# Optimization experiments

Hardware: AMD Instinct MI355X
Metric: run time of the kernel (lower is better)

Reference implementation:

```python
import jax, jax.numpy as jnp
import numpy as np

N = 8192
D_IN = 1024
D_OUT = 1024


def setup_inputs() -> dict:
    key = jax.random.key(0)
    k1, k2, k3, k4 = jax.random.split(key, 4)
    # param scales mimic reset_parameters: weight ~ U(-r, r), transfers ~ N(0, 0.001)
    r = np.sqrt(6.0 / (D_IN + D_OUT))
    x = jax.random.normal(k1, (N, D_IN), dtype=jnp.float32)
    weight = jax.random.uniform(k2, (D_IN, D_OUT), dtype=jnp.float32, minval=-r, maxval=r)
    transferi = jax.random.normal(k3, (D_IN, D_IN), dtype=jnp.float32) * 0.001
    transferj = jax.random.normal(k4, (D_IN, D_IN), dtype=jnp.float32) * 0.001
    return {"x": x, "weight": weight, "transferi": transferi, "transferj": transferj}


def reference(x, weight, transferi, transferj):
    # support = x @ W  -> [N, out]
    support = x @ weight
    # NOTE: the original torch code uses transferi for BOTH projections (transferj unused)
    x_i = x @ transferi            # [N, in]
    x_j = x @ transferi            # [N, in]
    scores = x_i @ x_j.T           # [N, N] inner-product attention, no scaling
    attn = jax.nn.softmax(scores, axis=1)
    return attn @ support          # [N, out]
```

## Files before the change

### kernel.cpp

```cpp
#include <hip/hip_runtime.h>
#include <hip/hip_bf16.h>
#include <cstddef>

#define NQ 8192
#define DD 1024

typedef __attribute__((ext_vector_type(8))) short s8v;
typedef __attribute__((ext_vector_type(8))) int i8v;
typedef __attribute__((ext_vector_type(4))) float f32x4;
typedef __attribute__((ext_vector_type(16))) float f32x16;

typedef const __attribute__((address_space(1))) unsigned int* gptr_t;
typedef __attribute__((address_space(3))) unsigned int* lptr_t;

#define SCALE_1_16 0x7B7B7B7Bu

__device__ inline unsigned short f2bf(float f) {
  union { float f; unsigned u; } v; v.f = f;
  unsigned r = (v.u + 0x7FFFu + ((v.u >> 16) & 1u)) >> 16;
  return (unsigned short)r;
}
__device__ inline float bits2f(unsigned u) {
  union { unsigned u; float f; } v; v.u = u;
  return v.f;
}

__device__ inline unsigned char f2e4m3(float x) {
  union { float f; unsigned u; } v; v.f = x;
  const unsigned s = (v.u >> 31) << 7;
  unsigned au = v.u & 0x7FFFFFFFu;
  if (au > 0x43E00000u) au = 0x43E00000u;
  if (au >= 0x3C800000u) {
    const unsigned rounded = au + 0x7FFFFu + ((au >> 20) & 1u);
    const unsigned e8 = ((rounded >> 23) & 0xFF) - 120u;
    const unsigned m8 = (rounded >> 20) & 7u;
    return (unsigned char)(s | (e8 << 3) | m8);
  } else {
    union { unsigned u; float f; } a; a.u = au;
    const unsigned q = (unsigned)rintf(a.f * 512.0f);
    return (unsigned char)(s | q);
  }
}

__device__ inline i8v make_i8v(int4 a, int4 b) {
  i8v v;
  v[0] = a.x; v[1] = a.y; v[2] = a.z; v[3] = a.w;
  v[4] = b.x; v[5] = b.y; v[6] = b.z; v[7] = b.w;
  return v;
}

template <int KDIM, int ASTR, int BSTR>
__device__ inline void mfma_core(const unsigned short* __restrict__ A,
                                 const unsigned short* __restrict__ B,
                                 int i0, int j0, int tid,
                                 unsigned short* AsU, unsigned short* BsU,
                                 f32x4 (&acc)[4][4]) {
  const int lane = tid & 63;
  const int w = tid >> 6;
  const int wr = (w >> 1) * 64;
  const int wc = (w & 1) * 64;
  const int l16 = lane & 15;
  const int lq = lane >> 4;
  const int srow = lane >> 3;
  const int scol = (((lane & 7) ^ (srow & 7)) * 8);

  for (int kk = 0; kk < KDIM; kk += 64) {
    __syncthreads();
#pragma unroll
    for (int t = 0; t < 4; t++) {
      const int r0 = w * 32 + t * 8;
      const unsigned short* g = &A[(size_t)(i0 + r0 + srow) * ASTR + kk + scol];
      __builtin_amdgcn_global_load_lds((gptr_t)(const void*)g,
                                       (lptr_t)(void*)&AsU[r0 * 64], 16, 0, 0);
    }
#pragma unroll
    for (int t = 0; t < 4; t++) {
      const int r0 = w * 32 + t * 8;
      const unsigned short* g = &B[(size_t)(j0 + r0 + srow) * BSTR + kk + scol];
      __builtin_amdgcn_global_load_lds((gptr_t)(const void*)g,
                                       (lptr_t)(void*)&BsU[r0 * 64], 16, 0, 0);
    }
    __syncthreads();

    const int h = l16 & 7;
    s8v af[4][2], bf[4][2];
#pragma unroll
    for (int t = 0; t < 4; t++)
#pragma unroll
      for (int s = 0; s < 2; s++) {
        const int ch = ((s * 4 + lq) ^ h) * 8;
        af[t][s] = *(const s8v*)&AsU[(wr + 16 * t + l16) * 64 + ch];
        bf[t][s] = *(const s8v*)&BsU[(wc + 16 * t + l16) * 64 + ch];
      }
#pragma unroll
    for (int s = 0; s < 2; s++)
#pragma unroll
      for (int a = 0; a < 4; a++)
#pragma unroll
        for (int b = 0; b < 4; b++)
          acc[a][b] = __builtin_amdgcn_mfma_f32_16x16x32_bf16(
              af[a][s], bf[b][s], acc[a][b], 0, 0, 0);
  }
}

__global__ void f32_to_bf16(const float* __restrict__ in,
                            unsigned short* __restrict__ out, int n4) {
  int i = (blockIdx.x * blockDim.x + threadIdx.x);
  if (i < n4) {
    const float4 v = *(const float4*)&in[i * 4];
    ushort4 o;
    o.x = f2bf(v.x); o.y = f2bf(v.y); o.z = f2bf(v.z); o.w = f2bf(v.w);
    *(ushort4*)&out[i * 4] = o;
  }
}

__global__ void zero_f32(float* __restrict__ p, int n) {
  const int i = blockIdx.x * blockDim.x + threadIdx.x;
  if (i < n) p[i] = 0.f;
}

__global__ void zero_f32v4(float* __restrict__ p, int n4) {
  const int i = blockIdx.x * blockDim.x + threadIdx.x;
  if (i < n4) *(float4*)&p[i * 4] = (float4){0.f, 0.f, 0.f, 0.f};
}

__global__ void transpose_cvt(const float* __restrict__ in,
                              unsigned short* __restrict__ out, int R, int C) {
  __shared__ float t[32][33];
  const int bx = blockIdx.x;
  const int by = blockIdx.y;
  const int x = threadIdx.x & 31;
  const int y = threadIdx.x >> 5;
#pragma unroll
  for (int i = 0; i < 32; i += 8)
    t[y + i][x] = in[(size_t)(by * 32 + y + i) * C + bx * 32 + x];
  __syncthreads();
#pragma unroll
  for (int i = 0; i < 32; i += 8)
    out[(size_t)(bx * 32 + y + i) * R + by * 32 + x] = f2bf(t[x][y + i]);
}

template <int NST, bool FP8OUT>
__global__ __launch_bounds__(256, 2)
void proj_gemm(const unsigned short* __restrict__ A,
               const unsigned short* __restrict__ BT,
               void* __restrict__ Cout) {
  __shared__ __align__(16) unsigned short As[128 * 64];
  __shared__ __align__(16) unsigned short Bs[128 * 64];
  const int tid = threadIdx.x;
  const int m0 = blockIdx.y * 128;
  const int n0 = blockIdx.x * 128;

  f32x4 acc[4][4];
#pragma unroll
  for (int a = 0; a < 4; a++)
#pragma unroll
    for (int b = 0; b < 4; b++) acc[a][b] = (f32x4){0.f, 0.f, 0.f, 0.f};

  mfma_core<DD, DD, DD>(A, BT, m0, n0, tid, As, Bs, acc);

  const int lane = tid & 63;
  const int w = tid >> 6;
  const int wr = (w >> 1) * 64, wc = (w & 1) * 64;
  const int l16 = lane & 15, lq = lane >> 4;
#pragma unroll
  for (int ti = 0; ti < 4; ti++)
#pragma unroll
    for (int r = 0; r < 4; r++) {
      const int row = m0 + wr + 16 * ti + lq * 4 + r;
#pragma unroll
      for (int tj = 0; tj < 4; tj++) {
        const int col = n0 + wc + 16 * tj + l16;
        if (FP8OUT) {
          ((unsigned char*)Cout)[(size_t)row * NST + col] =
              f2e4m3(acc[ti][tj][r] * 16.f);
        } else {
          ((unsigned short*)Cout)[(size_t)row * NST + col] = f2bf(acc[ti][tj][r]);
        }
      }
    }
}

__global__ __launch_bounds__(256, 3)
void qk_fp8(const unsigned char* __restrict__ xif,
            unsigned short* __restrict__ P,
            float* __restrict__ lsum) {
  __shared__ __align__(16) unsigned char AsF[128 * 64];
  __shared__ __align__(16) unsigned char BsF[128 * 64];
  __shared__ float lsums[128][65];
  const int tid = threadIdx.x;
  const int lane = tid & 63;
  const int w = tid >> 6;
  const int i0 = blockIdx.y * 128;
  const int j0 = blockIdx.x * 128;

  f32x16 acc[2][2];
#pragma unroll
  for (int a = 0; a < 2; a++)
#pragma unroll
    for (int b = 0; b < 2; b++)
#pragma unroll
      for (int r = 0; r < 16; r++) acc[a][b][r] = 0.f;

  const int srow = lane >> 2;
  const int slot = lane & 3;
  const int kb = lane >> 5;
  const int l31 = lane & 31;

  for (int kk = 0; kk < DD; kk += 64) {
    __syncthreads();
#pragma unroll
    for (int t = 0; t < 2; t++) {
      const int r = w * 32 + t * 16 + srow;
      const int c = slot ^ ((r >> 1) & 3);
      const unsigned char* ga = &xif[(size_t)(i0 + r) * DD + kk + c * 16];
      const unsigned char* gb = &xif[(size_t)(j0 + r) * DD + kk + c * 16];
      __builtin_amdgcn_global_load_lds((gptr_t)(const void*)ga,
                                       (lptr_t)(void*)&AsF[(w * 32 + t * 16) * 64],
                                       16, 0, 0);
      __builtin_amdgcn_global_load_lds((gptr_t)(const void*)gb,
                                       (lptr_t)(void*)&BsF[(w * 32 + t * 16) * 64],
                                       16, 0, 0);
    }
    __syncthreads();

    i8v af[2], bf[2];
#pragma unroll
    for (int mi = 0; mi < 2; mi++) {
      const int ar = (w >> 1) * 64 + mi * 32 + l31;
      const int sw = (ar >> 1) & 3;
      const int4 q0 = *(const int4*)&AsF[ar * 64 + ((2 * kb + 0) ^ sw) * 16];
      const int4 q1 = *(const int4*)&AsF[ar * 64 + ((2 * kb + 1) ^ sw) * 16];
      af[mi] = make_i8v(q0, q1);
    }
#pragma unroll
    for (int nj = 0; nj < 2; nj++) {
      const int br = (w & 1) * 64 + nj * 32 + l31;
      const int sw = (br >> 1) & 3;
      const int4 q0 = *(const int4*)&BsF[br * 64 + ((2 * kb + 0) ^ sw) * 16];
      const int4 q1 = *(const int4*)&BsF[br * 64 + ((2 * kb + 1) ^ sw) * 16];
      bf[nj] = make_i8v(q0, q1);
    }
#pragma unroll
    for (int mi = 0; mi < 2; mi++)
#pragma unroll
      for (int nj = 0; nj < 2; nj++)
        acc[mi][nj] = __builtin_amdgcn_mfma_scale_f32_32x32x64_f8f6f4(
            af[mi], bf[nj], acc[mi][nj], 0 , 0 ,
            0, SCALE_1_16, 0, SCALE_1_16);
  }

  const int mbase = (w >> 1) * 64;
  const int nbase = (w & 1) * 64;
  const int rowoff = 4 * (lane >> 5);
  const int cslot = (w & 1) * 32 + l31;
#pragma unroll
  for (int mi = 0; mi < 2; mi++)
#pragma unroll
    for (int r4 = 0; r4 < 4; r4++)
#pragma unroll
      for (int rr = 0; rr < 4; rr++) {
        const int reg = r4 * 4 + rr;
        const int rl = mbase + mi * 32 + rr + 8 * r4 + rowoff;
        const float p0 = __expf(acc[mi][0][reg]);
        const float p1 = __expf(acc[mi][1][reg]);
        const size_t base = (size_t)(i0 + rl) * NQ + j0 + nbase + l31;
        P[base]      = f2bf(p0);
        P[base + 32] = f2bf(p1);
        lsums[rl][cslot] = p0 + p1;
      }
  __syncthreads();
  if (tid < 128) {
    float s = 0.f;
#pragma unroll
    for (int c = 0; c < 64; c++) s += lsums[tid][c];
    atomicAdd(&lsum[i0 + tid], s);
  }
}

__global__ __launch_bounds__(256, 4)
void pv(const unsigned short* __restrict__ P,
        const unsigned short* __restrict__ supT,
        const float* __restrict__ lsum,
        float* __restrict__ out) {
  __shared__ __align__(16) unsigned short As[128 * 64];
  __shared__ __align__(16) unsigned short Bs[128 * 64];
  const int tid = threadIdx.x;
  const int i0 = blockIdx.x * 128;
  const int n0 = blockIdx.y * 128;
  const int k0 = blockIdx.z * (NQ / 2);

  f32x4 acc[4][4];
#pragma unroll
  for (int a = 0; a < 4; a++)
#pragma unroll
    for (int b = 0; b < 4; b++) acc[a][b] = (f32x4){0.f, 0.f, 0.f, 0.f};

  mfma_core<NQ / 2, NQ, NQ>(P + k0, supT + k0, i0, n0, tid, As, Bs, acc);

  const int lane = tid & 63;
  const int w = tid >> 6;
  const int wr = (w >> 1) * 64, wc = (w & 1) * 64;
  const int l16 = lane & 15, lq = lane >> 4;
#pragma unroll
  for (int ti = 0; ti < 4; ti++) {
#pragma unroll
    for (int r = 0; r < 4; r++) {
      const int row = i0 + wr + 16 * ti + lq * 4 + r;
      const float linv = 1.f / lsum[row];
#pragma unroll
      for (int tj = 0; tj < 4; tj++) {
        const int col = n0 + wc + 16 * tj + l16;
        atomicAdd(&out[(size_t)row * DD + col], acc[ti][tj][r] * linv);
      }
    }
  }
}

#define BM 64
#define BN 64
#define BK 16

__global__ __launch_bounds__(256, 4)
void gemm64(const float* __restrict__ A, const float* __restrict__ B,
            float* __restrict__ C, int M, int N, int K) {
  __shared__ __align__(16) float As[BK][BM + 4];
  __shared__ __align__(16) float Bs[BK][BN + 4];
  const int tid = threadIdx.x;
  const int tx = tid & 15;
  const int ty = tid >> 4;
  const int row0 = blockIdx.y * BM;
  const int col0 = blockIdx.x * BN;
  float acc[4][4] = {};
  for (int k0 = 0; k0 < K; k0 += BK) {
    {
      const int r = tid >> 2;
      const int c4 = (tid & 3) * 4;
      const float4 v = *(const float4*)&A[(size_t)(row0 + r) * K + k0 + c4];
      As[c4 + 0][r] = v.x; As[c4 + 1][r] = v.y;
      As[c4 + 2][r] = v.z; As[c4 + 3][r] = v.w;
    }
    {
      const int r = tid >> 4;
      const int c4 = (tid & 15) * 4;
      *(float4*)&Bs[r][c4] = *(const float4*)&B[(size_t)(k0 + r) * N + col0 + c4];
    }
    __syncthreads();
#pragma unroll
    for (int k = 0; k < BK; k++) {
      const float4 a = *(const float4*)&As[k][4 * ty];
      const float4 b = *(const float4*)&Bs[k][4 * tx];
      const float av[4] = {a.x, a.y, a.z, a.w};
      const float bv[4] = {b.x, b.y, b.z, b.w};
#pragma unroll
      for (int i = 0; i < 4; i++)
#pragma unroll
        for (int j = 0; j < 4; j++)
          acc[i][j] += av[i] * bv[j];
    }
    __syncthreads();
  }
#pragma unroll
  for (int i = 0; i < 4; i++) {
    float4 o = {acc[i][0], acc[i][1], acc[i][2], acc[i][3]};
    *(float4*)&C[(size_t)(row0 + 4 * ty + i) * N + col0 + 4 * tx] = o;
  }
}

#define IT 32
#define JT 128
#define KC 32
#define CC 128
#define NCH (DD / CC)

__global__ __launch_bounds__(256, 1)
void fused_attn(const float* __restrict__ xi, const float* __restrict__ sup,
                float* __restrict__ out) {
  __shared__ __align__(16) float XiI[KC][IT + 4];
  __shared__ __align__(16) float XiJ[KC][JT + 4];
  __shared__ __align__(16) float Ps[JT][IT + 4];
  __shared__ __align__(16) float Vs[JT][CC + 4];
  __shared__ float lsum[IT];
  const int tid = threadIdx.x;
  const int i0 = blockIdx.x * IT;
  const int ry = tid >> 5;
  const int cx = tid & 31;
  if (tid < IT) lsum[tid] = 0.f;
  float oacc[NCH][4][4];
#pragma unroll
  for (int ch = 0; ch < NCH; ch++)
#pragma unroll
    for (int i = 0; i < 4; i++)
#pragma unroll
      for (int j = 0; j < 4; j++) oacc[ch][i][j] = 0.f;
  for (int j0 = 0; j0 < NQ; j0 += JT) {
    float sacc[4][4] = {};
    for (int kc = 0; kc < DD; kc += KC) {
      __syncthreads();
      {
        const int r = tid >> 3;
        const int k4 = (tid & 7) * 4;
        const float4 v = *(const float4*)&xi[(size_t)(i0 + r) * DD + kc + k4];
        XiI[k4 + 0][r] = v.x; XiI[k4 + 1][r] = v.y;
        XiI[k4 + 2][r] = v.z; XiI[k4 + 3][r] = v.w;
      }
#pragma unroll
      for (int i = 0; i < 4; i++) {
        const int idx = tid + i * 256;
        const int r = idx >> 3;
        const int k4 = (idx & 7) * 4;
        const float4 v = *(const float4*)&xi[(size_t)(j0 + r) * DD + kc + k4];
        XiJ[k4 + 0][r] = v.x; XiJ[k4 + 1][r] = v.y;
        XiJ[k4 + 2][r] = v.z; XiJ[k4 + 3][r] = v.w;
      }
      __syncthreads();
#pragma unroll
      for (int k = 0; k < KC; k++) {
        const float4 a = *(const float4*)&XiI[k][4 * ry];
        const float4 b = *(const float4*)&XiJ[k][4 * cx];
        const float av[4] = {a.x, a.y, a.z, a.w};
        const float bv[4] = {b.x, b.y, b.z, b.w};
#pragma unroll
        for (int i = 0; i < 4; i++)
#pragma unroll
          for (int j = 0; j < 4; j++)
            sacc[i][j] += av[i] * bv[j];
      }
    }
    __syncthreads();
    float rsv[4] = {0.f, 0.f, 0.f, 0.f};
#pragma unroll
    for (int i = 0; i < 4; i++)
#pragma unroll
      for (int j = 0; j < 4; j++) {
        const float p = __expf(sacc[i][j]);
        Ps[4 * cx + j][4 * ry + i] = p;
        rsv[i] += p;
      }
#pragma unroll
    for (int m = 16; m >= 1; m >>= 1)
#pragma unroll
      for (int i = 0; i < 4; i++) rsv[i] += __shfl_xor(rsv[i], m);
    if (cx == 0) {
#pragma unroll
      for (int i = 0; i < 4; i++) lsum[4 * ry + i] += rsv[i];
    }
    for (int ch = 0; ch < NCH; ch++) {
      __syncthreads();
#pragma unroll
      for (int i = 0; i < 16; i++) {
        const int idx = tid + i * 256;
        const int r = idx >> 5;
        const int c4 = (idx & 31) * 4;
        *(float4*)&Vs[r][c4] =
            *(const float4*)&sup[(size_t)(j0 + r) * DD + ch * CC + c4];
      }
      __syncthreads();
#pragma unroll 4
      for (int jp = 0; jp < JT; jp++) {
        const float4 p = *(const float4*)&Ps[jp][4 * ry];
        const float4 v = *(const float4*)&Vs[jp][4 * cx];
        const float pvv[4] = {p.x, p.y, p.z, p.w};
        const float vv[4] = {v.x, v.y, v.z, v.w};
#pragma unroll
        for (int i = 0; i < 4; i++)
#pragma unroll
          for (int j = 0; j < 4; j++)
            oacc[ch][i][j] += pvv[i] * vv[j];
      }
    }
  }
  __syncthreads();
  float linv[4];
#pragma unroll
  for (int i = 0; i < 4; i++) linv[i] = 1.f / lsum[4 * ry + i];
#pragma unroll
  for (int ch = 0; ch < NCH; ch++)
#pragma unroll
    for (int i = 0; i < 4; i++) {
      float4 o = {oacc[ch][i][0] * linv[i], oacc[ch][i][1] * linv[i],
                  oacc[ch][i][2] * linv[i], oacc[ch][i][3] * linv[i]};
      *(float4*)&out[(size_t)(i0 + 4 * ry + i) * DD + ch * CC + 4 * cx] = o;
    }
}

extern "C" void kernel_launch(void* const* d_in, const int* in_sizes, int n_in,
                              void* d_out, int out_size, void* d_ws, size_t ws_size,
                              hipStream_t stream) {
  const float* x  = (const float*)d_in[0];
  const float* wt = (const float*)d_in[1];
  const float* ti = (const float*)d_in[2];
  float* out = (float*)d_out;

  char* ws = (char*)d_ws;
  const size_t MB = 1024 * 1024;
  const size_t NEED = 152 * MB + NQ * sizeof(float);

  if (ws_size >= NEED) {
    unsigned short* P    = (unsigned short*)ws;
    unsigned char*  xif  = (unsigned char*)(ws + 128 * MB);
    unsigned short* supT = (unsigned short*)(ws + 136 * MB);
    float* lsum          = (float*)(ws + 152 * MB);
    unsigned short* xb   = (unsigned short*)ws;
    unsigned short* tiT  = (unsigned short*)(ws + 16 * MB);
    unsigned short* wT   = (unsigned short*)(ws + 18 * MB);

    const int n4 = NQ * DD / 4;
    zero_f32v4<<<(n4 + 255) / 256, 256, 0, stream>>>(out, n4);
    zero_f32<<<NQ / 256, 256, 0, stream>>>(lsum, NQ);
    f32_to_bf16<<<(n4 + 255) / 256, 256, 0, stream>>>(x, xb, n4);
    transpose_cvt<<<dim3(32, 32), 256, 0, stream>>>(ti, tiT, DD, DD);
    transpose_cvt<<<dim3(32, 32), 256, 0, stream>>>(wt, wT, DD, DD);

    proj_gemm<DD, true><<<dim3(DD / 128, NQ / 128), 256, 0, stream>>>(xb, tiT, xif);
    proj_gemm<NQ, false><<<dim3(NQ / 128, DD / 128), 256, 0, stream>>>(wT, xb, supT);

    qk_fp8<<<dim3(NQ / 128, NQ / 128), 256, 0, stream>>>(xif, P, lsum);
    pv<<<dim3(NQ / 128, DD / 128, 2), 256, 0, stream>>>(P, supT, lsum, out);
  } else {
    float* xi32  = (float*)ws;
    float* sup32 = (float*)(ws + 32 * MB);
    dim3 ggrid(DD / BN, NQ / BM);
    gemm64<<<ggrid, 256, 0, stream>>>(x, ti, xi32, NQ, DD, DD);
    gemm64<<<ggrid, 256, 0, stream>>>(x, wt, sup32, NQ, DD, DD);
    fused_attn<<<NQ / IT, 256, 0, stream>>>(xi32, sup32, out);
  }
}
```

Baseline: 390.1 us.

## Store attention probabilities as offset FP8 and run PV in FP8 MFMA

The qk kernel now stores (exp(s)-1)*128 as e4m3 bytes instead of bf16 probabilities, which halves the P matrix traffic. The PV product runs on scaled fp8 MFMA against an fp8 copy of support. The removed constant term is added back through a per-column sum of support and an 8192 offset in the normaliser. This drops the out-zeroing kernel and the split-K atomics, at the cost of extra fp8 quantization error in both P and V.

```diff
diff --git a/kernel.cpp b/kernel.cpp
--- a/kernel.cpp
+++ b/kernel.cpp
@@ -14,6 +14,8 @@
 typedef __attribute__((address_space(3))) unsigned int* lptr_t;
 
 #define SCALE_1_16 0x7B7B7B7Bu
+#define SCALE_1_128 0x78787878u
+#define SCALE_1    0x7F7F7F7Fu
 
 __device__ inline unsigned short f2bf(float f) {
   union { float f; unsigned u; } v; v.f = f;
@@ -119,11 +121,6 @@
   if (i < n) p[i] = 0.f;
 }
 
-__global__ void zero_f32v4(float* __restrict__ p, int n4) {
-  const int i = blockIdx.x * blockDim.x + threadIdx.x;
-  if (i < n4) *(float4*)&p[i * 4] = (float4){0.f, 0.f, 0.f, 0.f};
-}
-
 __global__ void transpose_cvt(const float* __restrict__ in,
                               unsigned short* __restrict__ out, int R, int C) {
   __shared__ float t[32][33];
@@ -140,11 +137,11 @@
     out[(size_t)(bx * 32 + y + i) * R + by * 32 + x] = f2bf(t[x][y + i]);
 }
 
-template <int NST, bool FP8OUT>
+template <int NST, int OUTMODE>
 __global__ __launch_bounds__(256, 2)
 void proj_gemm(const unsigned short* __restrict__ A,
                const unsigned short* __restrict__ BT,
-               void* __restrict__ Cout) {
+               void* __restrict__ C1, void* __restrict__ C2) {
   __shared__ __align__(16) unsigned short As[128 * 64];
   __shared__ __align__(16) unsigned short Bs[128 * 64];
   const int tid = threadIdx.x;
@@ -171,19 +168,44 @@
 #pragma unroll
       for (int tj = 0; tj < 4; tj++) {
         const int col = n0 + wc + 16 * tj + l16;
-        if (FP8OUT) {
-          ((unsigned char*)Cout)[(size_t)row * NST + col] =
-              f2e4m3(acc[ti][tj][r] * 16.f);
+        const size_t idx = (size_t)row * NST + col;
+        const float v = acc[ti][tj][r];
+        if (OUTMODE == 1) {
+          ((unsigned char*)C1)[idx] = f2e4m3(v * 16.f);
         } else {
-          ((unsigned short*)Cout)[(size_t)row * NST + col] = f2bf(acc[ti][tj][r]);
+          ((unsigned short*)C1)[idx] = f2bf(v);
+          if (OUTMODE == 2) ((unsigned char*)C2)[idx] = f2e4m3(v);
         }
       }
     }
+}
+
+__global__ __launch_bounds__(256, 4)
+void colsum_bf16(const unsigned short* __restrict__ supT,
+                 float* __restrict__ colV) {
+  const int row = blockIdx.x;
+  const int tid = threadIdx.x;
+  const unsigned short* pr = &supT[(size_t)row * NQ];
+  float s = 0.f;
+#pragma unroll
+  for (int i = 0; i < 4; i++) {
+    const int4 q = *(const int4*)&pr[(size_t)(tid + i * 256) * 8];
+    s += bits2f((unsigned)q.x << 16) + bits2f((unsigned)q.x & 0xFFFF0000u);
+    s += bits2f((unsigned)q.y << 16) + bits2f((unsigned)q.y & 0xFFFF0000u);
+    s += bits2f((unsigned)q.z << 16) + bits2f((unsigned)q.z & 0xFFFF0000u);
+    s += bits2f((unsigned)q.w << 16) + bits2f((unsigned)q.w & 0xFFFF0000u);
+  }
+#pragma unroll
+  for (int m = 32; m >= 1; m >>= 1) s += __shfl_xor(s, m);
+  __shared__ float red[4];
+  if ((tid & 63) == 0) red[tid >> 6] = s;
+  __syncthreads();
+  if (tid == 0) colV[row] = red[0] + red[1] + red[2] + red[3];
 }
 
 __global__ __launch_bounds__(256, 3)
 void qk_fp8(const unsigned char* __restrict__ xif,
-            unsigned short* __restrict__ P,
+            unsigned char* __restrict__ Pd,
             float* __restrict__ lsum) {
   __shared__ __align__(16) unsigned char AsF[128 * 64];
   __shared__ __align__(16) unsigned char BsF[128 * 64];
@@ -265,9 +287,9 @@
         const float p0 = __expf(acc[mi][0][reg]);
         const float p1 = __expf(acc[mi][1][reg]);
         const size_t base = (size_t)(i0 + rl) * NQ + j0 + nbase + l31;
-        P[base]      = f2bf(p0);
-        P[base + 32] = f2bf(p1);
-        lsums[rl][cslot] = p0 + p1;
+        Pd[base]      = f2e4m3((p0 - 1.f) * 128.f);
+        Pd[base + 32] = f2e4m3((p1 - 1.f) * 128.f);
+        lsums[rl][cslot] = (p0 + p1) - 2.f;
       }
   __syncthreads();
   if (tid < 128) {
@@ -278,43 +300,95 @@
   }
 }
 
-__global__ __launch_bounds__(256, 4)
-void pv(const unsigned short* __restrict__ P,
-        const unsigned short* __restrict__ supT,
-        const float* __restrict__ lsum,
-        float* __restrict__ out) {
-  __shared__ __align__(16) unsigned short As[128 * 64];
-  __shared__ __align__(16) unsigned short Bs[128 * 64];
+__global__ __launch_bounds__(256, 2)
+void pv_fp8(const unsigned char* __restrict__ Pd,
+            const unsigned char* __restrict__ V8,
+            const float* __restrict__ lsum,
+            const float* __restrict__ colV,
+            float* __restrict__ out) {
+  __shared__ __align__(16) unsigned char AsF[128 * 64];
+  __shared__ __align__(16) unsigned char BsF[128 * 64];
   const int tid = threadIdx.x;
-  const int i0 = blockIdx.x * 128;
-  const int n0 = blockIdx.y * 128;
-  const int k0 = blockIdx.z * (NQ / 2);
-
-  f32x4 acc[4][4];
-#pragma unroll
-  for (int a = 0; a < 4; a++)
-#pragma unroll
-    for (int b = 0; b < 4; b++) acc[a][b] = (f32x4){0.f, 0.f, 0.f, 0.f};
-
-  mfma_core<NQ / 2, NQ, NQ>(P + k0, supT + k0, i0, n0, tid, As, Bs, acc);
-
   const int lane = tid & 63;
   const int w = tid >> 6;
-  const int wr = (w >> 1) * 64, wc = (w & 1) * 64;
-  const int l16 = lane & 15, lq = lane >> 4;
-#pragma unroll
-  for (int ti = 0; ti < 4; ti++) {
-#pragma unroll
-    for (int r = 0; r < 4; r++) {
-      const int row = i0 + wr + 16 * ti + lq * 4 + r;
-      const float linv = 1.f / lsum[row];
-#pragma unroll
-      for (int tj = 0; tj < 4; tj++) {
-        const int col = n0 + wc + 16 * tj + l16;
-        atomicAdd(&out[(size_t)row * DD + col], acc[ti][tj][r] * linv);
-      }
-    }
-  }
+  const int i0 = blockIdx.y * 128;
+  const int n0 = blockIdx.x * 128;
+
+  f32x16 acc[2][2];
+#pragma unroll
+  for (int a = 0; a < 2; a++)
+#pragma unroll
+    for (int b = 0; b < 2; b++)
+#pragma unroll
+      for (int r = 0; r < 16; r++) acc[a][b][r] = 0.f;
+
+  const int srow = lane >> 2;
+  const int slot = lane & 3;
+  const int kb = lane >> 5;
+  const int l31 = lane & 31;
+
+  for (int kk = 0; kk < NQ; kk += 64) {
+    __syncthreads();
+#pragma unroll
+    for (int t = 0; t < 2; t++) {
+      const int r = w * 32 + t * 16 + srow;
+      const int c = slot ^ ((r >> 1) & 3);
+      const unsigned char* ga = &Pd[(size_t)(i0 + r) * NQ + kk + c * 16];
+      const unsigned char* gb = &V8[(size_t)(n0 + r) * NQ + kk + c * 16];
+      __builtin_amdgcn_global_load_lds((gptr_t)(const void*)ga,
+                                       (lptr_t)(void*)&AsF[(w * 32 + t * 16) * 64],
+                                       16, 0, 0);
+      __builtin_amdgcn_global_load_lds((gptr_t)(const void*)gb,
+                                       (lptr_t)(void*)&BsF[(w * 32 + t * 16) * 64],
+                                       16, 0, 0);
+    }
+    __syncthreads();
+
+    i8v af[2], bf[2];
+#pragma unroll
+    for (int mi = 0; mi < 2; mi++) {
+      const int ar = (w >> 1) * 64 + mi * 32 + l31;
+      const int sw = (ar >> 1) & 3;
+      const int4 q0 = *(const int4*)&AsF[ar * 64 + ((2 * kb + 0) ^ sw) * 16];
+      const int4 q1 = *(const int4*)&AsF[ar * 64 + ((2 * kb + 1) ^ sw) * 16];
+      af[mi] = make_i8v(q0, q1);
+    }
+#pragma unroll
+    for (int nj = 0; nj < 2; nj++) {
+      const int br = (w & 1) * 64 + nj * 32 + l31;
+      const int sw = (br >> 1) & 3;
+      const int4 q0 = *(const int4*)&BsF[br * 64 + ((2 * kb + 0) ^ sw) * 16];
+      const int4 q1 = *(const int4*)&BsF[br * 64 + ((2 * kb + 1) ^ sw) * 16];
+      bf[nj] = make_i8v(q0, q1);
+    }
+#pragma unroll
+    for (int mi = 0; mi < 2; mi++)
+#pragma unroll
+      for (int nj = 0; nj < 2; nj++)
+        acc[mi][nj] = __builtin_amdgcn_mfma_scale_f32_32x32x64_f8f6f4(
+            af[mi], bf[nj], acc[mi][nj], 0 , 0 ,
+            0, SCALE_1_128, 0, SCALE_1);
+  }
+
+  const int mbase = (w >> 1) * 64;
+  const int nbase = (w & 1) * 64;
+  const int rowoff = 4 * (lane >> 5);
+  const int c0 = n0 + nbase + l31;
+  const float cv0 = colV[c0];
+  const float cv1 = colV[c0 + 32];
+#pragma unroll
+  for (int mi = 0; mi < 2; mi++)
+#pragma unroll
+    for (int r4 = 0; r4 < 4; r4++)
+#pragma unroll
+      for (int rr = 0; rr < 4; rr++) {
+        const int reg = r4 * 4 + rr;
+        const int rl = mbase + mi * 32 + rr + 8 * r4 + rowoff;
+        const int row = i0 + rl;
+        const float linv = 1.f / (8192.f + lsum[row]);
+        out[(size_t)row * DD + c0]      = (cv0 + acc[mi][0][reg]) * linv;
+        out[(size_t)row * DD + c0 + 32] = (cv1 + acc[mi][1][reg]) * linv;
+      }
 }
 
 #define BM 64
@@ -497,26 +571,31 @@
   const size_t NEED = 152 * MB + NQ * sizeof(float);
 
   if (ws_size >= NEED) {
-    unsigned short* P    = (unsigned short*)ws;
-    unsigned char*  xif  = (unsigned char*)(ws + 128 * MB);
-    unsigned short* supT = (unsigned short*)(ws + 136 * MB);
-    float* lsum          = (float*)(ws + 152 * MB);
-    unsigned short* xb   = (unsigned short*)ws;
-    unsigned short* tiT  = (unsigned short*)(ws + 16 * MB);
-    unsigned short* wT   = (unsigned short*)(ws + 18 * MB);
+    unsigned char*  Pd    = (unsigned char*)ws;
+    unsigned char*  supT8 = (unsigned char*)(ws + 64 * MB);
+    float*          colV  = (float*)(ws + 72 * MB);
+    unsigned char*  xif   = (unsigned char*)(ws + 128 * MB);
+    unsigned short* supT  = (unsigned short*)(ws + 136 * MB);
+    float*          lsum  = (float*)(ws + 152 * MB);
+    unsigned short* xb    = (unsigned short*)ws;
+    unsigned short* tiT   = (unsigned short*)(ws + 16 * MB);
+    unsigned short* wT    = (unsigned short*)(ws + 18 * MB);
 
     const int n4 = NQ * DD / 4;
-    zero_f32v4<<<(n4 + 255) / 256, 256, 0, stream>>>(out, n4);
     zero_f32<<<NQ / 256, 256, 0, stream>>>(lsum, NQ);
     f32_to_bf16<<<(n4 + 255) / 256, 256, 0, stream>>>(x, xb, n4);
     transpose_cvt<<<dim3(32, 32), 256, 0, stream>>>(ti, tiT, DD, DD);
     transpose_cvt<<<dim3(32, 32), 256, 0, stream>>>(wt, wT, DD, DD);
 
-    proj_gemm<DD, true><<<dim3(DD / 128, NQ / 128), 256, 0, stream>>>(xb, tiT, xif);
-    proj_gemm<NQ, false><<<dim3(NQ / 128, DD / 128), 256, 0, stream>>>(wT, xb, supT);
-
-    qk_fp8<<<dim3(NQ / 128, NQ / 128), 256, 0, stream>>>(xif, P, lsum);
-    pv<<<dim3(NQ / 128, DD / 128, 2), 256, 0, stream>>>(P, supT, lsum, out);
+    proj_gemm<DD, 1><<<dim3(DD / 128, NQ / 128), 256, 0, stream>>>(
+        xb, tiT, xif, nullptr);
+    proj_gemm<NQ, 2><<<dim3(NQ / 128, DD / 128), 256, 0, stream>>>(
+        wT, xb, supT, supT8);
+    colsum_bf16<<<DD, 256, 0, stream>>>(supT, colV);
+
+    qk_fp8<<<dim3(NQ / 128, NQ / 128), 256, 0, stream>>>(xif, Pd, lsum);
+    pv_fp8<<<dim3(DD / 128, NQ / 128), 256, 0, stream>>>(Pd, supT8, lsum,
+                                                         colV, out);
   } else {
     float* xi32  = (float*)ws;
     float* sup32 = (float*)(ws + 32 * MB);
```

Result: slower. 753.6 us (+93.2%).

## Replace split-K atomic PV GEMM with larger-tile full-K double-buffered kernel

Applied to the files above, without the earlier changes.

The P·V kernel now uses 256x128 output tiles with full K per block, double-buffered LDS staging through global_load_lds with an XOR swizzle, and 16x16x32 bf16 MFMAs. Because each block owns its whole output tile, results are written with plain stores instead of atomics, and the zeroing pass over the output is dropped. The larger tile raises reuse of P and supT per load. In exchange the grid shrinks to 256 blocks at occupancy 1, which may underfill the GPU and leave less latency hiding.

```diff
diff --git a/kernel.cpp b/kernel.cpp
--- a/kernel.cpp
+++ b/kernel.cpp
@@ -119,11 +119,6 @@
   if (i < n) p[i] = 0.f;
 }
 
-__global__ void zero_f32v4(float* __restrict__ p, int n4) {
-  const int i = blockIdx.x * blockDim.x + threadIdx.x;
-  if (i < n4) *(float4*)&p[i * 4] = (float4){0.f, 0.f, 0.f, 0.f};
-}
-
 __global__ void transpose_cvt(const float* __restrict__ in,
                               unsigned short* __restrict__ out, int R, int C) {
   __shared__ float t[32][33];
@@ -278,43 +273,92 @@
   }
 }
 
-__global__ __launch_bounds__(256, 4)
-void pv(const unsigned short* __restrict__ P,
-        const unsigned short* __restrict__ supT,
-        const float* __restrict__ lsum,
-        float* __restrict__ out) {
-  __shared__ __align__(16) unsigned short As[128 * 64];
-  __shared__ __align__(16) unsigned short Bs[128 * 64];
+__global__ __launch_bounds__(256, 1)
+void pv_fat(const unsigned short* __restrict__ P,
+            const unsigned short* __restrict__ supT,
+            const float* __restrict__ lsum,
+            float* __restrict__ out) {
+  __shared__ __align__(16) unsigned short As[2][256 * 64];
+  __shared__ __align__(16) unsigned short Bs[2][128 * 64];
   const int tid = threadIdx.x;
-  const int i0 = blockIdx.x * 128;
-  const int n0 = blockIdx.y * 128;
-  const int k0 = blockIdx.z * (NQ / 2);
-
-  f32x4 acc[4][4];
-#pragma unroll
-  for (int a = 0; a < 4; a++)
-#pragma unroll
-    for (int b = 0; b < 4; b++) acc[a][b] = (f32x4){0.f, 0.f, 0.f, 0.f};
-
-  mfma_core<NQ / 2, NQ, NQ>(P + k0, supT + k0, i0, n0, tid, As, Bs, acc);
-
   const int lane = tid & 63;
   const int w = tid >> 6;
-  const int wr = (w >> 1) * 64, wc = (w & 1) * 64;
-  const int l16 = lane & 15, lq = lane >> 4;
-#pragma unroll
-  for (int ti = 0; ti < 4; ti++) {
+  const int l16 = lane & 15;
+  const int lq = lane >> 4;
+  const int srow = lane >> 3;
+  const int scol = ((lane & 7) ^ srow) * 8;
+  const int i0 = blockIdx.y * 256;
+  const int n0 = blockIdx.x * 128;
+
+  f32x4 acc[4][8];
+#pragma unroll
+  for (int a = 0; a < 4; a++)
+#pragma unroll
+    for (int b = 0; b < 8; b++) acc[a][b] = (f32x4){0.f, 0.f, 0.f, 0.f};
+
+  auto stage = [&](int buf, int t) {
+    const int kk = t * 64;
+#pragma unroll
+    for (int q = 0; q < 8; q++) {
+      const int r0 = w * 64 + q * 8;
+      const unsigned short* g = &P[(size_t)(i0 + r0 + srow) * NQ + kk + scol];
+      __builtin_amdgcn_global_load_lds((gptr_t)(const void*)g,
+                                       (lptr_t)(void*)&As[buf][r0 * 64], 16, 0, 0);
+    }
+#pragma unroll
+    for (int q = 0; q < 4; q++) {
+      const int r0 = w * 32 + q * 8;
+      const unsigned short* g = &supT[(size_t)(n0 + r0 + srow) * NQ + kk + scol];
+      __builtin_amdgcn_global_load_lds((gptr_t)(const void*)g,
+                                       (lptr_t)(void*)&Bs[buf][r0 * 64], 16, 0, 0);
+    }
+  };
+
+  stage(0, 0);
+  asm volatile("s_waitcnt vmcnt(0)" ::: "memory");
+  __syncthreads();
+
+  const int h = l16 & 7;
+  int cur = 0;
+#pragma unroll 1
+  for (int t = 0; t < NQ / 64; t++) {
+    if (t < NQ / 64 - 1) stage(cur ^ 1, t + 1);
+    const unsigned short* Ac = &As[cur][0];
+    const unsigned short* Bc = &Bs[cur][0];
+#pragma unroll
+    for (int s = 0; s < 2; s++) {
+      const int ch = ((s * 4 + lq) ^ h) * 8;
+      s8v af[4], bf[8];
+#pragma unroll
+      for (int a = 0; a < 4; a++)
+        af[a] = *(const s8v*)&Ac[(w * 64 + 16 * a + l16) * 64 + ch];
+#pragma unroll
+      for (int b = 0; b < 8; b++)
+        bf[b] = *(const s8v*)&Bc[(16 * b + l16) * 64 + ch];
+#pragma unroll
+      for (int a = 0; a < 4; a++)
+#pragma unroll
+        for (int b = 0; b < 8; b++)
+          acc[a][b] = __builtin_amdgcn_mfma_f32_16x16x32_bf16(
+              af[a], bf[b], acc[a][b], 0, 0, 0);
+    }
+    asm volatile("s_waitcnt vmcnt(0)" ::: "memory");
+    __syncthreads();
+    cur ^= 1;
+  }
+
+#pragma unroll
+  for (int a = 0; a < 4; a++)
 #pragma unroll
     for (int r = 0; r < 4; r++) {
-      const int row = i0 + wr + 16 * ti + lq * 4 + r;
+      const int row = i0 + w * 64 + 16 * a + lq * 4 + r;
       const float linv = 1.f / lsum[row];
 #pragma unroll
-      for (int tj = 0; tj < 4; tj++) {
-        const int col = n0 + wc + 16 * tj + l16;
-        atomicAdd(&out[(size_t)row * DD + col], acc[ti][tj][r] * linv);
-      }
-    }
-  }
+      for (int b = 0; b < 8; b++) {
+        const int col = n0 + 16 * b + l16;
+        out[(size_t)row * DD + col] = acc[a][b][r] * linv;
+      }
+    }
 }
 
 #define BM 64
@@ -506,7 +550,6 @@
     unsigned short* wT   = (unsigned short*)(ws + 18 * MB);
 
     const int n4 = NQ * DD / 4;
-    zero_f32v4<<<(n4 + 255) / 256, 256, 0, stream>>>(out, n4);
     zero_f32<<<NQ / 256, 256, 0, stream>>>(lsum, NQ);
     f32_to_bf16<<<(n4 + 255) / 256, 256, 0, stream>>>(x, xb, n4);
     transpose_cvt<<<dim3(32, 32), 256, 0, stream>>>(ti, tiT, DD, DD);
@@ -516,7 +559,7 @@
     proj_gemm<NQ, false><<<dim3(NQ / 128, DD / 128), 256, 0, stream>>>(wT, xb, supT);
 
     qk_fp8<<<dim3(NQ / 128, NQ / 128), 256, 0, stream>>>(xif, P, lsum);
-    pv<<<dim3(NQ / 128, DD / 128, 2), 256, 0, stream>>>(P, supT, lsum, out);
+    pv_fat<<<dim3(DD / 128, NQ / 256), 256, 0, stream>>>(P, supT, lsum, out);
   } else {
     float* xi32  = (float*)ws;
     float* sup32 = (float*)(ws + 32 * MB);
```

Measured after the change: 436.3 us. 1.12x slower.

## Double-buffer LDS tiles in GEMM kernels and drop split-K atomics in PV

Applied to the files above, without the earlier changes.

Converts the shared MFMA inner loop and the fp8 QK kernel to double-buffered LDS staging, so the global-to-LDS loads for the next K tile are issued before computing on the current tile. This hides load latency behind the MFMAs and cuts the number of barriers per tile. The PV kernel drops its 2-way split-K, writing results directly instead of using atomicAdd, which also removes the output zeroing kernel. In exchange LDS use doubles, launch bounds fall to 2 blocks per SM, and the PV grid halves, which lowers occupancy and parallelism.

```diff
diff --git a/kernel.cpp b/kernel.cpp
--- a/kernel.cpp
+++ b/kernel.cpp
@@ -50,11 +50,14 @@
 }
 
 template <int KDIM, int ASTR, int BSTR>
-__device__ inline void mfma_core(const unsigned short* __restrict__ A,
-                                 const unsigned short* __restrict__ B,
-                                 int i0, int j0, int tid,
-                                 unsigned short* AsU, unsigned short* BsU,
-                                 f32x4 (&acc)[4][4]) {
+__device__ inline void mfma_core_db(const unsigned short* __restrict__ A,
+                                    const unsigned short* __restrict__ B,
+                                    int i0, int j0, int tid,
+                                    unsigned short* __restrict__ As0,
+                                    unsigned short* __restrict__ As1,
+                                    unsigned short* __restrict__ Bs0,
+                                    unsigned short* __restrict__ Bs1,
+                                    f32x4 (&acc)[4][4]) {
   const int lane = tid & 63;
   const int w = tid >> 6;
   const int wr = (w >> 1) * 64;
@@ -64,33 +67,43 @@
   const int srow = lane >> 3;
   const int scol = (((lane & 7) ^ (srow & 7)) * 8);
 
-  for (int kk = 0; kk < KDIM; kk += 64) {
-    __syncthreads();
+  auto stage = [&](unsigned short* dA, unsigned short* dB, int kk) {
 #pragma unroll
     for (int t = 0; t < 4; t++) {
       const int r0 = w * 32 + t * 8;
       const unsigned short* g = &A[(size_t)(i0 + r0 + srow) * ASTR + kk + scol];
       __builtin_amdgcn_global_load_lds((gptr_t)(const void*)g,
-                                       (lptr_t)(void*)&AsU[r0 * 64], 16, 0, 0);
+                                       (lptr_t)(void*)&dA[r0 * 64], 16, 0, 0);
     }
 #pragma unroll
     for (int t = 0; t < 4; t++) {
       const int r0 = w * 32 + t * 8;
       const unsigned short* g = &B[(size_t)(j0 + r0 + srow) * BSTR + kk + scol];
       __builtin_amdgcn_global_load_lds((gptr_t)(const void*)g,
-                                       (lptr_t)(void*)&BsU[r0 * 64], 16, 0, 0);
-    }
-    __syncthreads();
-
-    const int h = l16 & 7;
+                                       (lptr_t)(void*)&dB[r0 * 64], 16, 0, 0);
+    }
+  };
+
+  stage(As0, Bs0, 0);
+  asm volatile("s_waitcnt vmcnt(0)" ::: "memory");
+  __syncthreads();
+
+  const int h = l16 & 7;
+  unsigned short* curA = As0;
+  unsigned short* curB = Bs0;
+  unsigned short* nxtA = As1;
+  unsigned short* nxtB = Bs1;
+#pragma unroll 1
+  for (int t = 0; t < KDIM / 64; t++) {
+    if (t < KDIM / 64 - 1) stage(nxtA, nxtB, (t + 1) * 64);
     s8v af[4][2], bf[4][2];
 #pragma unroll
-    for (int t = 0; t < 4; t++)
+    for (int q = 0; q < 4; q++)
 #pragma unroll
       for (int s = 0; s < 2; s++) {
         const int ch = ((s * 4 + lq) ^ h) * 8;
-        af[t][s] = *(const s8v*)&AsU[(wr + 16 * t + l16) * 64 + ch];
-        bf[t][s] = *(const s8v*)&BsU[(wc + 16 * t + l16) * 64 + ch];
+        af[q][s] = *(const s8v*)&curA[(wr + 16 * q + l16) * 64 + ch];
+        bf[q][s] = *(const s8v*)&curB[(wc + 16 * q + l16) * 64 + ch];
       }
 #pragma unroll
     for (int s = 0; s < 2; s++)
@@ -100,6 +113,10 @@
         for (int b = 0; b < 4; b++)
           acc[a][b] = __builtin_amdgcn_mfma_f32_16x16x32_bf16(
               af[a][s], bf[b][s], acc[a][b], 0, 0, 0);
+    asm volatile("s_waitcnt vmcnt(0)" ::: "memory");
+    __syncthreads();
+    unsigned short* tA = curA; curA = nxtA; nxtA = tA;
+    unsigned short* tB = curB; curB = nxtB; nxtB = tB;
   }
 }
 
@@ -119,11 +136,6 @@
   if (i < n) p[i] = 0.f;
 }
 
-__global__ void zero_f32v4(float* __restrict__ p, int n4) {
-  const int i = blockIdx.x * blockDim.x + threadIdx.x;
-  if (i < n4) *(float4*)&p[i * 4] = (float4){0.f, 0.f, 0.f, 0.f};
-}
-
 __global__ void transpose_cvt(const float* __restrict__ in,
                               unsigned short* __restrict__ out, int R, int C) {
   __shared__ float t[32][33];
@@ -145,8 +157,8 @@
 void proj_gemm(const unsigned short* __restrict__ A,
                const unsigned short* __restrict__ BT,
                void* __restrict__ Cout) {
-  __shared__ __align__(16) unsigned short As[128 * 64];
-  __shared__ __align__(16) unsigned short Bs[128 * 64];
+  __shared__ __align__(16) unsigned short As[2][128 * 64];
+  __shared__ __align__(16) unsigned short Bs[2][128 * 64];
   const int tid = threadIdx.x;
   const int m0 = blockIdx.y * 128;
   const int n0 = blockIdx.x * 128;
@@ -157,7 +169,7 @@
 #pragma unroll
     for (int b = 0; b < 4; b++) acc[a][b] = (f32x4){0.f, 0.f, 0.f, 0.f};
 
-  mfma_core<DD, DD, DD>(A, BT, m0, n0, tid, As, Bs, acc);
+  mfma_core_db<DD, DD, DD>(A, BT, m0, n0, tid, As[0], As[1], Bs[0], Bs[1], acc);
 
   const int lane = tid & 63;
   const int w = tid >> 6;
@@ -181,12 +193,12 @@
     }
 }
 
-__global__ __launch_bounds__(256, 3)
+__global__ __launch_bounds__(256, 2)
 void qk_fp8(const unsigned char* __restrict__ xif,
             unsigned short* __restrict__ P,
             float* __restrict__ lsum) {
-  __shared__ __align__(16) unsigned char AsF[128 * 64];
-  __shared__ __align__(16) unsigned char BsF[128 * 64];
+  __shared__ __align__(16) unsigned char AsF[2][128 * 64];
+  __shared__ __align__(16) unsigned char BsF[2][128 * 64];
   __shared__ float lsums[128][65];
   const int tid = threadIdx.x;
   const int lane = tid & 63;
@@ -207,8 +219,7 @@
   const int kb = lane >> 5;
   const int l31 = lane & 31;
 
-  for (int kk = 0; kk < DD; kk += 64) {
-    __syncthreads();
+  auto stage = [&](unsigned char* dA, unsigned char* dB, int kk) {
 #pragma unroll
     for (int t = 0; t < 2; t++) {
       const int r = w * 32 + t * 16 + srow;
@@ -216,29 +227,41 @@
       const unsigned char* ga = &xif[(size_t)(i0 + r) * DD + kk + c * 16];
       const unsigned char* gb = &xif[(size_t)(j0 + r) * DD + kk + c * 16];
       __builtin_amdgcn_global_load_lds((gptr_t)(const void*)ga,
-                                       (lptr_t)(void*)&AsF[(w * 32 + t * 16) * 64],
+                                       (lptr_t)(void*)&dA[(w * 32 + t * 16) * 64],
                                        16, 0, 0);
       __builtin_amdgcn_global_load_lds((gptr_t)(const void*)gb,
-                                       (lptr_t)(void*)&BsF[(w * 32 + t * 16) * 64],
+                                       (lptr_t)(void*)&dB[(w * 32 + t * 16) * 64],
                                        16, 0, 0);
     }
-    __syncthreads();
+  };
+
+  stage(AsF[0], BsF[0], 0);
+  asm volatile("s_waitcnt vmcnt(0)" ::: "memory");
+  __syncthreads();
+
+  unsigned char* curA = AsF[0];
+  unsigned char* curB = BsF[0];
+  unsigned char* nxtA = AsF[1];
+  unsigned char* nxtB = BsF[1];
+#pragma unroll 1
+  for (int t = 0; t < DD / 64; t++) {
+    if (t < DD / 64 - 1) stage(nxtA, nxtB, (t + 1) * 64);
 
     i8v af[2], bf[2];
 #pragma unroll
     for (int mi = 0; mi < 2; mi++) {
       const int ar = (w >> 1) * 64 + mi * 32 + l31;
       const int sw = (ar >> 1) & 3;
-      const int4 q0 = *(const int4*)&AsF[ar * 64 + ((2 * kb + 0) ^ sw) * 16];
-      const int4 q1 = *(const int4*)&AsF[ar * 64 + ((2 * kb + 1) ^ sw) * 16];
+      const int4 q0 = *(const int4*)&curA[ar * 64 + ((2 * kb + 0) ^ sw) * 16];
+      const int4 q1 = *(const int4*)&curA[ar * 64 + ((2 * kb + 1) ^ sw) * 16];
       af[mi] = make_i8v(q0, q1);
     }
 #pragma unroll
     for (int nj = 0; nj < 2; nj++) {
       const int br = (w & 1) * 64 + nj * 32 + l31;
       const int sw = (br >> 1) & 3;
-      const int4 q0 = *(const int4*)&BsF[br * 64 + ((2 * kb + 0) ^ sw) * 16];
-      const int4 q1 = *(const int4*)&BsF[br * 64 + ((2 * kb + 1) ^ sw) * 16];
+      const int4 q0 = *(const int4*)&curB[br * 64 + ((2 * kb + 0) ^ sw) * 16];
+      const int4 q1 = *(const int4*)&curB[br * 64 + ((2 * kb + 1) ^ sw) * 16];
       bf[nj] = make_i8v(q0, q1);
     }
 #pragma unroll
@@ -248,6 +271,11 @@
         acc[mi][nj] = __builtin_amdgcn_mfma_scale_f32_32x32x64_f8f6f4(
             af[mi], bf[nj], acc[mi][nj], 0 , 0 ,
             0, SCALE_1_16, 0, SCALE_1_16);
+
+    asm volatile("s_waitcnt vmcnt(0)" ::: "memory");
+    __syncthreads();
+    unsigned char* tA = curA; curA = nxtA; nxtA = tA;
+    unsigned char* tB = curB; curB = nxtB; nxtB = tB;
   }
 
   const int mbase = (w >> 1) * 64;
@@ -278,17 +306,16 @@
   }
 }
 
-__global__ __launch_bounds__(256, 4)
+__global__ __launch_bounds__(256, 2)
 void pv(const unsigned short* __restrict__ P,
         const unsigned short* __restrict__ supT,
         const float* __restrict__ lsum,
         float* __restrict__ out) {
-  __shared__ __align__(16) unsigned short As[128 * 64];
-  __shared__ __align__(16) unsigned short Bs[128 * 64];
+  __shared__ __align__(16) unsigned short As[2][128 * 64];
+  __shared__ __align__(16) unsigned short Bs[2][128 * 64];
   const int tid = threadIdx.x;
   const int i0 = blockIdx.x * 128;
   const int n0 = blockIdx.y * 128;
-  const int k0 = blockIdx.z * (NQ / 2);
 
   f32x4 acc[4][4];
 #pragma unroll
@@ -296,7 +323,8 @@
 #pragma unroll
     for (int b = 0; b < 4; b++) acc[a][b] = (f32x4){0.f, 0.f, 0.f, 0.f};
 
-  mfma_core<NQ / 2, NQ, NQ>(P + k0, supT + k0, i0, n0, tid, As, Bs, acc);
+  mfma_core_db<NQ, NQ, NQ>(P, supT, i0, n0, tid, As[0], As[1], Bs[0], Bs[1],
+                           acc);
 
   const int lane = tid & 63;
   const int w = tid >> 6;
@@ -311,7 +339,7 @@
 #pragma unroll
       for (int tj = 0; tj < 4; tj++) {
         const int col = n0 + wc + 16 * tj + l16;
-        atomicAdd(&out[(size_t)row * DD + col], acc[ti][tj][r] * linv);
+        out[(size_t)row * DD + col] = acc[ti][tj][r] * linv;
       }
     }
   }
@@ -506,7 +534,6 @@
     unsigned short* wT   = (unsigned short*)(ws + 18 * MB);
 
     const int n4 = NQ * DD / 4;
-    zero_f32v4<<<(n4 + 255) / 256, 256, 0, stream>>>(out, n4);
     zero_f32<<<NQ / 256, 256, 0, stream>>>(lsum, NQ);
     f32_to_bf16<<<(n4 + 255) / 256, 256, 0, stream>>>(x, xb, n4);
     transpose_cvt<<<dim3(32, 32), 256, 0, stream>>>(ti, tiT, DD, DD);
@@ -516,7 +543,7 @@
     proj_gemm<NQ, false><<<dim3(NQ / 128, DD / 128), 256, 0, stream>>>(wT, xb, supT);
 
     qk_fp8<<<dim3(NQ / 128, NQ / 128), 256, 0, stream>>>(xif, P, lsum);
-    pv<<<dim3(NQ / 128, DD / 128, 2), 256, 0, stream>>>(P, supT, lsum, out);
+    pv<<<dim3(NQ / 128, DD / 128), 256, 0, stream>>>(P, supT, lsum, out);
   } else {
     float* xi32  = (float*)ws;
     float* sup32 = (float*)(ws + 32 * MB);
```

Result: faster. 370.4 us (-5.1%).
